# Optimization experiments

Hardware: AMD Instinct MI355X
Metric: run time of the kernel (lower is better)

The kernel has to match this reference:

```python
import jax, jax.numpy as jnp
import numpy as np

EPS = 1e-5

def conv(x, w, stride=1, pad=0, groups=1):
    # x: NCHW, w: OIHW
    return jax.lax.conv_general_dilated(
        x, w, window_strides=(stride, stride),
        padding=[(pad, pad), (pad, pad)],
        dimension_numbers=("NCHW", "OIHW", "NCHW"),
        feature_group_count=groups)

def bn_eval(x, gamma, beta, mean, var):
    scale = (gamma / jnp.sqrt(var + EPS))[None, :, None, None]
    shift = (beta - mean * gamma / jnp.sqrt(var + EPS))[None, :, None, None]
    return x * scale + shift

def setup_inputs() -> dict:
    key = jax.random.key(0)
    ks = jax.random.split(key, 12)
    B, Cin, H, W = 32, 64, 56, 56
    hidden, red, Cout, K = 384, 16, 64, 3
    f32 = jnp.float32
    x = jax.random.normal(ks[0], (B, Cin, H, W), dtype=f32)
    w_exp = jax.random.normal(ks[1], (hidden, Cin, 3, 3), dtype=f32) * 0.05
    w_dw  = jax.random.normal(ks[2], (hidden, 1, K, K), dtype=f32) * 0.1
    w_se1 = jax.random.normal(ks[3], (red, hidden, 1, 1), dtype=f32) * 0.05
    w_se2 = jax.random.normal(ks[4], (hidden, red, 1, 1), dtype=f32) * 0.1
    w_pw  = jax.random.normal(ks[5], (Cout, hidden, 1, 1), dtype=f32) * 0.05
    def bn_params(k, c):
        k1, k2 = jax.random.split(k)
        return (jnp.ones((c,), f32), jnp.zeros((c,), f32),
                jax.random.normal(k1, (c,), dtype=f32) * 0.01,
                jax.random.uniform(k2, (c,), dtype=f32, minval=0.5, maxval=1.5))
    g1, b1, m1, v1 = bn_params(ks[6], hidden)
    g2, b2, m2, v2 = bn_params(ks[7], hidden)
    g3, b3, m3, v3 = bn_params(ks[8], Cout)
    return dict(x=x, w_exp=w_exp, g1=g1, b1=b1, m1=m1, v1=v1,
                w_dw=w_dw, g2=g2, b2=b2, m2=m2, v2=v2,
                w_se1=w_se1, w_se2=w_se2, w_pw=w_pw,
                g3=g3, b3=b3, m3=m3, v3=v3)

def reference(x, w_exp, g1, b1, m1, v1, w_dw, g2, b2, m2, v2,
              w_se1, w_se2, w_pw, g3, b3, m3, v3):
    hidden = w_exp.shape[0]
    # expand conv (3x3) + BN + SiLU
    h = jax.nn.silu(bn_eval(conv(x, w_exp, stride=1, pad=1), g1, b1, m1, v1))
    # depthwise conv + BN + SiLU
    d = jax.nn.silu(bn_eval(conv(h, w_dw, stride=1, pad=1, groups=hidden), g2, b2, m2, v2))
    # squeeze-excitation: global avg pool -> 1x1 -> SiLU -> 1x1 -> sigmoid -> scale
    s = jnp.mean(d, axis=(2, 3), keepdims=True)            # [B, hidden, 1, 1]
    s = jax.nn.silu(conv(s, w_se1))
    s = jax.nn.sigmoid(conv(s, w_se2))
    d = d * s
    # pointwise projection + BN
    y = bn_eval(conv(d, w_pw), g3, b3, m3, v3)
    # eval mode: stochastic_depth is identity; quant_skip == (identity-quantized) input
    return y + x
```

## Files before the change

kernel.cpp:

```cpp
#include <hip/hip_runtime.h>

typedef unsigned short u16;
typedef unsigned int u32;
typedef __attribute__((ext_vector_type(2))) u32 u32x2;
typedef __attribute__((ext_vector_type(4))) u32 u32x4;
typedef __attribute__((ext_vector_type(4))) float f32x4;
typedef __attribute__((ext_vector_type(8))) short s16x8;

#define DEV __device__ __forceinline__

DEV float bflo(u32 u){ union{u32 i; float f;} c; c.i = u << 16; return c.f; }
DEV float bfhi(u32 u){ union{u32 i; float f;} c; c.i = u & 0xffff0000u; return c.f; }
DEV u16 f2b(float f){
  union{float f; u32 u;} c; c.f = f;
  u32 u = c.u;
  u32 r = (u + 0x7fffu + ((u >> 16) & 1u)) >> 16;
  return (u16)r;
}
DEV float fsilu(float v){ return v / (1.f + __expf(-v)); }

constexpr int Bn = 32, Cin = 64, H = 56, Wd = 56, HID = 384, CO = 64;
constexpr int HW = H * Wd;
constexpr float EPS = 1e-5f;

constexpr int XROW = 72 * 64;
constexpr int WTAP = 128 * 64;
constexpr int WOCT = 9 * WTAP;

__global__ __launch_bounds__(256) void k_prep_wbn(
    const float* __restrict__ w,
    const float* __restrict__ g1, const float* __restrict__ b1,
    const float* __restrict__ m1, const float* __restrict__ v1,
    const float* __restrict__ g3, const float* __restrict__ b3,
    const float* __restrict__ m3, const float* __restrict__ v3,
    u16* __restrict__ wt,
    float* __restrict__ sc1, float* __restrict__ sh1,
    float* __restrict__ sc3, float* __restrict__ sh3)
{
  const int blk = blockIdx.x;
  if (blk < 864) {
    int t = blk * 256 + threadIdx.x;
    int octile = t / WOCT, r = t - octile * WOCT;
    int tap = r / WTAP, r2 = r - tap * WTAP;
    int ocl = r2 >> 6, col = r2 & 63;
    int physo = col >> 3, j = col & 7;
    int olog = physo ^ (ocl & 7);
    int ic = olog * 8 + j;
    int oc = octile * 128 + ocl;
    wt[t] = f2b(w[(oc * Cin + ic) * 9 + tap]);
  } else {
    for (int t = threadIdx.x; t < HID; t += 256) {
      float sc = g1[t] * rsqrtf(v1[t] + EPS);
      sc1[t] = sc;
      sh1[t] = b1[t] - m1[t] * sc;
    }
    if (threadIdx.x < CO) {
      int t = threadIdx.x;
      float sc = g3[t] * rsqrtf(v3[t] + EPS);
      sc3[t] = sc;
      sh3[t] = b3[t] - m3[t] * sc;
    }
  }
}

__global__ __launch_bounds__(256, 2) void k_expand_mfma(
    const float* __restrict__ x, const u16* __restrict__ wt,
    const float* __restrict__ sc1, const float* __restrict__ sh1,
    u16* __restrict__ h, int b0)
{
  __shared__ u16 sB[4 * XROW];
  __shared__ u16 sA[WTAP];
  const int tid = threadIdx.x;
  const int ypair = blockIdx.x, b = blockIdx.y;
  const int gb = b0 + b;
  const int y0 = ypair * 2;
  const int wave = tid >> 6, ln = tid & 63;
  const int wm = wave >> 1, wn = wave & 1;
  const int lane15 = ln & 15, quad = ln >> 4;

  {
    u32x4 z = {0, 0, 0, 0};
    #pragma unroll
    for (int i = 0; i < 18; ++i)
      *(u32x4*)&sB[(i * 256 + tid) * 8] = z;
  }
  __syncthreads();
  {
    const int ic = tid & 63, xq = tid >> 6;
    #pragma unroll
    for (int r = 0; r < 4; ++r) {
      const int y = y0 + r - 1;
      if (y >= 0 && y < H) {
        const float* xp = x + ((size_t)(gb * Cin + ic) * H + y) * Wd + xq * 14;
        float vals[14];
        #pragma unroll
        for (int t = 0; t < 14; ++t) vals[t] = xp[t];
        u16* rowp = &sB[r * XROW];
        #pragma unroll
        for (int t = 0; t < 14; ++t) {
          int slot = xq * 14 + t + 1;
          int pos = slot * 64 + (((ic >> 3) ^ (slot & 7)) << 3) + (ic & 7);
          rowp[pos] = f2b(vals[t]);
        }
      }
    }
  }

  const int y = y0 + wn;

  for (int octile = 0; octile < 3; ++octile) {
    f32x4 acc[4][4];
    #pragma unroll
    for (int ms = 0; ms < 4; ++ms)
      #pragma unroll
      for (int ns = 0; ns < 4; ++ns) acc[ms][ns] = (f32x4){0.f, 0.f, 0.f, 0.f};

    const u16* wsrc = wt + (size_t)octile * WOCT;
    for (int tap = 0; tap < 9; ++tap) {
      __syncthreads();
      #pragma unroll
      for (int it = 0; it < 4; ++it) {
        int i = it * 256 + tid;
        *(u32x4*)&sA[i * 8] = *(const u32x4*)&wsrc[tap * WTAP + i * 8];
      }
      __syncthreads();
      const int dy = tap / 3, dx = tap - dy * 3;
      #pragma unroll
      for (int kk = 0; kk < 2; ++kk) {
        s16x8 af[4], bf[4];
        #pragma unroll
        for (int ms = 0; ms < 4; ++ms) {
          int ocl = wm * 64 + ms * 16 + lane15;
          int po = (kk * 4 + quad) ^ (ocl & 7);
          af[ms] = *(const s16x8*)&sA[ocl * 64 + po * 8];
        }
        #pragma unroll
        for (int ns = 0; ns < 4; ++ns) {
          int row = wn + dy;
          int slot = ns * 16 + lane15 + dx;
          int po = (kk * 4 + quad) ^ (slot & 7);
          bf[ns] = *(const s16x8*)&sB[(row * 72 + slot) * 64 + po * 8];
        }
        #pragma unroll
        for (int ms = 0; ms < 4; ++ms)
          #pragma unroll
          for (int ns = 0; ns < 4; ++ns)
            acc[ms][ns] = __builtin_amdgcn_mfma_f32_16x16x32_bf16(
                af[ms], bf[ns], acc[ms][ns], 0, 0, 0);
      }
    }

    #pragma unroll
    for (int ms = 0; ms < 4; ++ms) {
      int oc0 = octile * 128 + wm * 64 + ms * 16 + quad * 4;
      f32x4 sc = *(const f32x4*)&sc1[oc0];
      f32x4 sh = *(const f32x4*)&sh1[oc0];
      float scr[4] = {sc.x, sc.y, sc.z, sc.w};
      float shr[4] = {sh.x, sh.y, sh.z, sh.w};
      #pragma unroll
      for (int ns = 0; ns < 4; ++ns) {
        int xg = ns * 16 + lane15;
        if (xg < Wd) {
          float av[4] = {acc[ms][ns].x, acc[ms][ns].y, acc[ms][ns].z, acc[ms][ns].w};
          #pragma unroll
          for (int r = 0; r < 4; ++r) {
            float val = fsilu(av[r] * scr[r] + shr[r]);
            h[((size_t)(b * HID + oc0 + r) * H + y) * Wd + xg] = f2b(val);
          }
        }
      }
    }
  }
}

__global__ __launch_bounds__(256) void k_dw(
    const u16* __restrict__ h, const float* __restrict__ wdw,
    const float* __restrict__ g2, const float* __restrict__ b2,
    const float* __restrict__ m2, const float* __restrict__ v2,
    u16* __restrict__ d, float* __restrict__ mean)
{
  __shared__ float red[4];
  const int tid = threadIdx.x;
  const int c = blockIdx.x, b = blockIdx.y;
  const u32* hp32 = (const u32*)(h + (size_t)(b * HID + c) * HW);

  float wv[9];
  #pragma unroll
  for (int t = 0; t < 9; ++t) wv[t] = wdw[c * 9 + t];
  const float sc = g2[c] * rsqrtf(v2[c] + EPS);
  const float sh = b2[c] - m2[c] * sc;

  float lsum = 0.f;
  if (tid < 224) {
    const int row = tid >> 2, seg = tid & 3;
    const int px0 = seg * 14, w0 = px0 >> 1;

    float v[3][16];
    #pragma unroll
    for (int r3 = 0; r3 < 3; ++r3) {
      int rr = row + r3 - 1;
      bool ok = (rr >= 0) && (rr < 56);
      const u32* rp = hp32 + rr * 28;
      v[r3][0] = (ok && seg > 0) ? bfhi(rp[w0 - 1]) : 0.f;
      #pragma unroll
      for (int t = 0; t < 7; ++t) {
        u32 wd = ok ? rp[w0 + t] : 0u;
        v[r3][1 + 2 * t] = bflo(wd);
        v[r3][2 + 2 * t] = bfhi(wd);
      }
      v[r3][15] = (ok && seg < 3) ? bflo(rp[w0 + 7]) : 0.f;
    }

    u32 pk[7];
    #pragma unroll
    for (int t = 0; t < 7; ++t) {
      float o2[2];
      #pragma unroll
      for (int e = 0; e < 2; ++e) {
        int j = 2 * t + e;
        float s = 0.f;
        #pragma unroll
        for (int r3 = 0; r3 < 3; ++r3)
          #pragma unroll
          for (int dx = 0; dx < 3; ++dx)
            s += v[r3][j + dx] * wv[r3 * 3 + dx];
        float val = fsilu(s * sc + sh);
        lsum += val;
        o2[e] = val;
      }
      pk[t] = (u32)f2b(o2[0]) | ((u32)f2b(o2[1]) << 16);
    }
    u32* dp32 = (u32*)(d + (size_t)(b * HID + c) * HW) + row * 28 + w0;
    #pragma unroll
    for (int t = 0; t < 7; ++t) dp32[t] = pk[t];
  }

  #pragma unroll
  for (int off = 32; off > 0; off >>= 1) lsum += __shfl_down(lsum, off);
  if ((tid & 63) == 0) red[tid >> 6] = lsum;
  __syncthreads();
  if (tid == 0)
    mean[b * HID + c] = (red[0] + red[1] + red[2] + red[3]) * (1.f / 3136.f);
}

__global__ __launch_bounds__(256) void k_se(
    const float* __restrict__ mean, const float* __restrict__ w1,
    const float* __restrict__ w2, float* __restrict__ sfac)
{
  __shared__ float sm[HID];
  __shared__ float ps[16 * 17];
  __shared__ float s1[16];
  const int b = blockIdx.x, tid = threadIdx.x;
  for (int c = tid; c < HID; c += 256) sm[c] = mean[b * HID + c];
  __syncthreads();
  int r = tid >> 4, j = tid & 15;
  float p = 0.f;
  for (int c = j; c < HID; c += 16) p += sm[c] * w1[r * HID + c];
  ps[r * 17 + j] = p;
  __syncthreads();
  if (tid < 16) {
    float s = 0.f;
    #pragma unroll
    for (int q = 0; q < 16; ++q) s += ps[tid * 17 + q];
    s1[tid] = fsilu(s);
  }
  __syncthreads();
  for (int c = tid; c < HID; c += 256) {
    float s = 0.f;
    #pragma unroll
    for (int q = 0; q < 16; ++q) s += s1[q] * w2[c * 16 + q];
    sfac[b * HID + c] = 1.f / (1.f + __expf(-s));
  }
}

constexpr int PWP = 392;

__global__ __launch_bounds__(256, 2) void k_pw_mfma(
    const u16* __restrict__ d, const float* __restrict__ sfac,
    const float* __restrict__ wpw,
    const float* __restrict__ sc3, const float* __restrict__ sh3,
    const float* __restrict__ x, float* __restrict__ out, int b0)
{
  __shared__ u16 sAw[64 * PWP];
  __shared__ u32 dtw[4 * 1024];
  const int tid = threadIdx.x;
  const int b = blockIdx.y, gb = b0 + b;
  const int p0 = blockIdx.x * 256;
  const int wave = tid >> 6, ln = tid & 63;
  const int lane15 = ln & 15, quad = ln >> 4;

  {
    for (int i = tid; i < 6144; i += 256) {
      int e = i * 4, co = e / 384, k = e - co * 384;
      f32x4 wv = *(const f32x4*)&wpw[e];
      f32x4 sf = *(const f32x4*)&sfac[b * HID + k];
      float s3 = sc3[co];
      u32x2 pk;
      pk.x = (u32)f2b(wv.x * sf.x * s3) | ((u32)f2b(wv.y * sf.y * s3) << 16);
      pk.y = (u32)f2b(wv.z * sf.z * s3) | ((u32)f2b(wv.w * sf.w * s3) << 16);
      *(u32x2*)&sAw[co * PWP + k] = pk;
    }
  }
  __syncthreads();

  f32x4 acc[4][4];
  #pragma unroll
  for (int ms = 0; ms < 4; ++ms)
    #pragma unroll
    for (int ns = 0; ns < 4; ++ns) acc[ms][ns] = (f32x4){0.f, 0.f, 0.f, 0.f};

  const int cpair8 = ln >> 3;
  const int pxo = (ln & 7) * 8;
  const int swz = ln & 3;
  const int pbase = p0 + wave * 64;
  u32* mydt = &dtw[wave * 1024];
  const bool ld_ok = (pbase + pxo + 8 <= HW);
  const u16* dbase = d + (size_t)b * HID * HW + pbase + pxo;

  u32x4 pr0[2], pr1[2];
  #pragma unroll
  for (int ci = 0; ci < 2; ++ci) {
    pr0[ci] = (u32x4){0,0,0,0}; pr1[ci] = (u32x4){0,0,0,0};
    if (ld_ok) {
      int c = 2 * (ci * 8 + cpair8);
      const u16* dpp = dbase + (size_t)c * HW;
      pr0[ci] = *(const u32x4*)dpp;
      pr1[ci] = *(const u32x4*)(dpp + HW);
    }
  }

  for (int ks = 0; ks < 12; ++ks) {
    #pragma unroll
    for (int ci = 0; ci < 2; ++ci) {
      int k4 = ci * 2 + (cpair8 >> 2);
      u32* w0 = &mydt[pxo * 16 + ((k4 ^ swz) << 2) + (cpair8 & 3)];
      u32x4 r0 = pr0[ci], r1 = pr1[ci];
      w0[0 * 16] = (r0.x & 0xffffu) | (r1.x << 16);
      w0[1 * 16] = (r0.x >> 16)     | (r1.x & 0xffff0000u);
      w0[2 * 16] = (r0.y & 0xffffu) | (r1.y << 16);
      w0[3 * 16] = (r0.y >> 16)     | (r1.y & 0xffff0000u);
      w0[4 * 16] = (r0.z & 0xffffu) | (r1.z << 16);
      w0[5 * 16] = (r0.z >> 16)     | (r1.z & 0xffff0000u);
      w0[6 * 16] = (r0.w & 0xffffu) | (r1.w << 16);
      w0[7 * 16] = (r0.w >> 16)     | (r1.w & 0xffff0000u);
    }
    if (ks < 11) {
      #pragma unroll
      for (int ci = 0; ci < 2; ++ci) {
        if (ld_ok) {
          int c = (ks + 1) * 32 + 2 * (ci * 8 + cpair8);
          const u16* dpp = dbase + (size_t)c * HW;
          pr0[ci] = *(const u32x4*)dpp;
          pr1[ci] = *(const u32x4*)(dpp + HW);
        }
      }
    }
    const int k0 = ks * 32;
    s16x8 af[4], bf[4];
    #pragma unroll
    for (int ms = 0; ms < 4; ++ms) {
      int ocl = ms * 16 + lane15;
      af[ms] = *(const s16x8*)&sAw[ocl * PWP + k0 + quad * 8];
    }
    #pragma unroll
    for (int ns = 0; ns < 4; ++ns) {
      int pxl = ns * 16 + lane15;
      int p4 = quad ^ ((pxl >> 3) & 3);
      bf[ns] = *(const s16x8*)((const u16*)mydt + pxl * 32 + p4 * 8);
    }
    #pragma unroll
    for (int ms = 0; ms < 4; ++ms)
      #pragma unroll
      for (int ns = 0; ns < 4; ++ns)
        acc[ms][ns] = __builtin_amdgcn_mfma_f32_16x16x32_bf16(
            af[ms], bf[ns], acc[ms][ns], 0, 0, 0);
  }

  #pragma unroll
  for (int ns = 0; ns < 4; ++ns) {
    int p = pbase + ns * 16 + lane15;
    if (p < HW) {
      #pragma unroll
      for (int ms = 0; ms < 4; ++ms) {
        int co0 = ms * 16 + quad * 4;
        float av[4] = {acc[ms][ns].x, acc[ms][ns].y, acc[ms][ns].z, acc[ms][ns].w};
        #pragma unroll
        for (int r = 0; r < 4; ++r) {
          size_t idx = (size_t)(gb * CO + co0 + r) * HW + p;
          out[idx] = av[r] + sh3[co0 + r] + x[idx];
        }
      }
    }
  }
}

extern "C" void kernel_launch(void* const* d_in, const int* in_sizes, int n_in,
                              void* d_out, int out_size, void* d_ws, size_t ws_size,
                              hipStream_t stream)
{
  (void)in_sizes; (void)n_in; (void)out_size;
  const float* x     = (const float*)d_in[0];
  const float* w_exp = (const float*)d_in[1];
  const float* g1 = (const float*)d_in[2];
  const float* b1 = (const float*)d_in[3];
  const float* m1 = (const float*)d_in[4];
  const float* v1 = (const float*)d_in[5];
  const float* w_dw = (const float*)d_in[6];
  const float* g2 = (const float*)d_in[7];
  const float* b2 = (const float*)d_in[8];
  const float* m2 = (const float*)d_in[9];
  const float* v2 = (const float*)d_in[10];
  const float* w_se1 = (const float*)d_in[11];
  const float* w_se2 = (const float*)d_in[12];
  const float* w_pw  = (const float*)d_in[13];
  const float* g3 = (const float*)d_in[14];
  const float* b3 = (const float*)d_in[15];
  const float* m3 = (const float*)d_in[16];
  const float* v3 = (const float*)d_in[17];

  const size_t perB = (size_t)HID * HW * 2 * 2 + HID * 8;
  const size_t fixed = 221184 * 2 + HID * 8 + CO * 8;
  int bc = Bn;
  while (bc > 1 && fixed + (size_t)bc * perB > ws_size) bc >>= 1;

  u16* wt = (u16*)d_ws;
  float* sc1 = (float*)(wt + 221184);
  float* sh1 = sc1 + HID;
  float* sc3 = sh1 + HID;
  float* sh3 = sc3 + CO;
  u16* h  = (u16*)(sh3 + CO);
  u16* dd = h + (size_t)bc * HID * HW;
  float* mean = (float*)(dd + (size_t)bc * HID * HW);
  float* sfac = mean + (size_t)bc * HID;

  k_prep_wbn<<<865, 256, 0, stream>>>(w_exp, g1, b1, m1, v1, g3, b3, m3, v3,
                                      wt, sc1, sh1, sc3, sh3);

  for (int b0 = 0; b0 < Bn; b0 += bc) {
    k_expand_mfma<<<dim3(28, bc), 256, 0, stream>>>(x, wt, sc1, sh1, h, b0);
    k_dw<<<dim3(HID, bc), 256, 0, stream>>>(h, w_dw, g2, b2, m2, v2, dd, mean);
    k_se<<<bc, 256, 0, stream>>>(mean, w_se1, w_se2, sfac);
    k_pw_mfma<<<dim3(13, bc), 256, 0, stream>>>(dd, sfac, w_pw, sc3, sh3,
                                                x, (float*)d_out, b0);
  }
}
```

Measured before the change: 279.5 us.

## Use direct global-to-LDS weight loads, raise expand occupancy, two rows per dw thread

The expand conv now loads each weight tap straight into LDS with global_load_lds, so the data no longer passes through registers, and its launch bound asks for 3 blocks per CU instead of 2. The depthwise kernel now computes two output rows per thread from four loaded input rows, with 128 threads per block, which reuses overlapping input rows and cuts redundant global loads. Risks: the higher occupancy target may cause register spills in the MFMA kernel, and the direct LDS copy needs the per-wave 512-element layout to match the swizzled layout the fragment reads expect.

```diff
diff --git a/kernel.cpp b/kernel.cpp
--- a/kernel.cpp
+++ b/kernel.cpp
@@ -18,6 +18,11 @@
   return (u16)r;
 }
 DEV float fsilu(float v){ return v / (1.f + __expf(-v)); }
+
+#define GLD_LDS16(gsrc, ldst)                                                  \
+  __builtin_amdgcn_global_load_lds(                                            \
+      (const __attribute__((address_space(1))) u32*)(gsrc),                    \
+      (__attribute__((address_space(3))) u32*)(ldst), 16, 0, 0)
 
 constexpr int Bn = 32, Cin = 64, H = 56, Wd = 56, HID = 384, CO = 64;
 constexpr int HW = H * Wd;
@@ -63,7 +68,7 @@
   }
 }
 
-__global__ __launch_bounds__(256, 2) void k_expand_mfma(
+__global__ __launch_bounds__(256, 3) void k_expand_mfma(
     const float* __restrict__ x, const u16* __restrict__ wt,
     const float* __restrict__ sc1, const float* __restrict__ sh1,
     u16* __restrict__ h, int b0)
@@ -118,10 +123,13 @@
     const u16* wsrc = wt + (size_t)octile * WOCT;
     for (int tap = 0; tap < 9; ++tap) {
       __syncthreads();
-      #pragma unroll
-      for (int it = 0; it < 4; ++it) {
-        int i = it * 256 + tid;
-        *(u32x4*)&sA[i * 8] = *(const u32x4*)&wsrc[tap * WTAP + i * 8];
+      {
+        const u16* src = wsrc + tap * WTAP;
+        #pragma unroll
+        for (int it = 0; it < 4; ++it) {
+          int off = (wave * 4 + it) * 512;
+          GLD_LDS16(src + off + ln * 8, &sA[off]);
+        }
       }
       __syncthreads();
       const int dy = tap / 3, dx = tap - dy * 3;
@@ -173,13 +181,13 @@
   }
 }
 
-__global__ __launch_bounds__(256) void k_dw(
+__global__ __launch_bounds__(128) void k_dw(
     const u16* __restrict__ h, const float* __restrict__ wdw,
     const float* __restrict__ g2, const float* __restrict__ b2,
     const float* __restrict__ m2, const float* __restrict__ v2,
     u16* __restrict__ d, float* __restrict__ mean)
 {
-  __shared__ float red[4];
+  __shared__ float red[2];
   const int tid = threadIdx.x;
   const int c = blockIdx.x, b = blockIdx.y;
   const u32* hp32 = (const u32*)(h + (size_t)(b * HID + c) * HW);
@@ -191,48 +199,53 @@
   const float sh = b2[c] - m2[c] * sc;
 
   float lsum = 0.f;
-  if (tid < 224) {
-    const int row = tid >> 2, seg = tid & 3;
-    const int px0 = seg * 14, w0 = px0 >> 1;
-
-    float v[3][16];
-    #pragma unroll
-    for (int r3 = 0; r3 < 3; ++r3) {
-      int rr = row + r3 - 1;
+  if (tid < 112) {
+    const int rp = tid >> 2, seg = tid & 3;
+    const int w0 = seg * 7;
+    const int r0 = rp * 2;
+
+    float v[4][16];
+    #pragma unroll
+    for (int r4 = 0; r4 < 4; ++r4) {
+      int rr = r0 + r4 - 1;
       bool ok = (rr >= 0) && (rr < 56);
-      const u32* rp = hp32 + rr * 28;
-      v[r3][0] = (ok && seg > 0) ? bfhi(rp[w0 - 1]) : 0.f;
+      const u32* rpt = hp32 + rr * 28;
+      v[r4][0] = (ok && seg > 0) ? bfhi(rpt[w0 - 1]) : 0.f;
       #pragma unroll
       for (int t = 0; t < 7; ++t) {
-        u32 wd = ok ? rp[w0 + t] : 0u;
-        v[r3][1 + 2 * t] = bflo(wd);
-        v[r3][2 + 2 * t] = bfhi(wd);
-      }
-      v[r3][15] = (ok && seg < 3) ? bflo(rp[w0 + 7]) : 0.f;
-    }
-
-    u32 pk[7];
-    #pragma unroll
-    for (int t = 0; t < 7; ++t) {
-      float o2[2];
-      #pragma unroll
-      for (int e = 0; e < 2; ++e) {
-        int j = 2 * t + e;
-        float s = 0.f;
-        #pragma unroll
-        for (int r3 = 0; r3 < 3; ++r3)
+        u32 wd = ok ? rpt[w0 + t] : 0u;
+        v[r4][1 + 2 * t] = bflo(wd);
+        v[r4][2 + 2 * t] = bfhi(wd);
+      }
+      v[r4][15] = (ok && seg < 3) ? bflo(rpt[w0 + 7]) : 0.f;
+    }
+
+    u32* dp32 = (u32*)(d + (size_t)(b * HID + c) * HW);
+    #pragma unroll
+    for (int orow = 0; orow < 2; ++orow) {
+      u32 pk[7];
+      #pragma unroll
+      for (int t = 0; t < 7; ++t) {
+        float o2[2];
+        #pragma unroll
+        for (int e = 0; e < 2; ++e) {
+          int j = 2 * t + e;
+          float s = 0.f;
           #pragma unroll
-          for (int dx = 0; dx < 3; ++dx)
-            s += v[r3][j + dx] * wv[r3 * 3 + dx];
-        float val = fsilu(s * sc + sh);
-        lsum += val;
-        o2[e] = val;
-      }
-      pk[t] = (u32)f2b(o2[0]) | ((u32)f2b(o2[1]) << 16);
-    }
-    u32* dp32 = (u32*)(d + (size_t)(b * HID + c) * HW) + row * 28 + w0;
-    #pragma unroll
-    for (int t = 0; t < 7; ++t) dp32[t] = pk[t];
+          for (int r3 = 0; r3 < 3; ++r3)
+            #pragma unroll
+            for (int dx = 0; dx < 3; ++dx)
+              s += v[orow + r3][j + dx] * wv[r3 * 3 + dx];
+          float val = fsilu(s * sc + sh);
+          lsum += val;
+          o2[e] = val;
+        }
+        pk[t] = (u32)f2b(o2[0]) | ((u32)f2b(o2[1]) << 16);
+      }
+      u32* op = dp32 + (r0 + orow) * 28 + w0;
+      #pragma unroll
+      for (int t = 0; t < 7; ++t) op[t] = pk[t];
+    }
   }
 
   #pragma unroll
@@ -240,7 +253,7 @@
   if ((tid & 63) == 0) red[tid >> 6] = lsum;
   __syncthreads();
   if (tid == 0)
-    mean[b * HID + c] = (red[0] + red[1] + red[2] + red[3]) * (1.f / 3136.f);
+    mean[b * HID + c] = (red[0] + red[1]) * (1.f / 3136.f);
 }
 
 __global__ __launch_bounds__(256) void k_se(
@@ -438,7 +451,7 @@
 
   for (int b0 = 0; b0 < Bn; b0 += bc) {
     k_expand_mfma<<<dim3(28, bc), 256, 0, stream>>>(x, wt, sc1, sh1, h, b0);
-    k_dw<<<dim3(HID, bc), 256, 0, stream>>>(h, w_dw, g2, b2, m2, v2, dd, mean);
+    k_dw<<<dim3(HID, bc), 128, 0, stream>>>(h, w_dw, g2, b2, m2, v2, dd, mean);
     k_se<<<bc, 256, 0, stream>>>(mean, w_se1, w_se2, sfac);
     k_pw_mfma<<<dim3(13, bc), 256, 0, stream>>>(dd, sfac, w_pw, sc3, sh3,
                                                 x, (float*)d_out, b0);
```

Result: slower. 313.9 us (+12.3%).
